# Kernel optimization log

Measured on AMD Instinct MI355X. Metric: run time of the kernel, lower is better.

The kernel has to match this reference:

```python
import jax, jax.numpy as jnp
import numpy as np

E = 1024  # embedding_size
H = 16    # multi_head_num


def setup_inputs() -> dict:
    key = jax.random.key(0)
    ks = jax.random.split(key, 9)
    B, N = 4, 1024
    s = 1.0 / np.sqrt(E)
    return {
        "x": jax.random.normal(ks[0], (B, N, E), dtype=jnp.float32),
        "Wq": jax.random.normal(ks[1], (E, E), dtype=jnp.float32) * s,
        "bq": jax.random.normal(ks[2], (E,), dtype=jnp.float32) * 0.02,
        "Wk": jax.random.normal(ks[3], (E, E), dtype=jnp.float32) * s,
        "bk": jax.random.normal(ks[4], (E,), dtype=jnp.float32) * 0.02,
        "Wv": jax.random.normal(ks[5], (E, E), dtype=jnp.float32) * s,
        "bv": jax.random.normal(ks[6], (E,), dtype=jnp.float32) * 0.02,
        "Wo": jax.random.normal(ks[7], (E, E), dtype=jnp.float32) * s,
        "bo": jax.random.normal(ks[8], (E,), dtype=jnp.float32) * 0.02,
    }


def reference(x, Wq, bq, Wk, bk, Wv, bv, Wo, bo):
    B, N, _ = x.shape
    d = E // H

    def heads(y):  # [B,N,E] -> [B,H,N,d]
        return y.reshape(B, N, H, d).transpose(0, 2, 1, 3)

    q = heads(x @ Wq.T + bq)
    k = heads(x @ Wk.T + bk)
    v = heads(x @ Wv.T + bv)

    energy = jnp.einsum('bhqd,bhkd->bhqk', q, k)
    # NOTE: module divides by sqrt(E) AFTER softmax (faithful to source)
    scaling = jnp.asarray(E, x.dtype) ** 0.5
    att = jax.nn.softmax(energy, axis=-1) / scaling
    out = jnp.einsum('bhal,bhlv->bhav', att, v)
    out = out.transpose(0, 2, 1, 3).reshape(B, N, E)
    return out @ Wo.T + bo
```

## Files before the change

### kernel.cpp

```cpp
#include <hip/hip_runtime.h>
#include <hip/hip_bf16.h>


typedef __bf16 bf16x8 __attribute__((ext_vector_type(8)));
typedef __bf16 bf16x4 __attribute__((ext_vector_type(4)));
typedef float  f32x4  __attribute__((ext_vector_type(4)));

#define LOG2E 1.44269504f

__device__ __forceinline__ void glds16(const __bf16* g, __bf16* l) {
  __builtin_amdgcn_global_load_lds(
      (const __attribute__((address_space(1))) void*)g,
      (__attribute__((address_space(3))) void*)l, 16, 0, 0);
}

__global__ __launch_bounds__(256) void cvt_f32_bf16(const float* __restrict__ in,
                                                    __bf16* __restrict__ out, int n4) {
  int i = blockIdx.x * 256 + threadIdx.x;
  if (i < n4) {
    float4 v = *(const float4*)(in + (size_t)i * 4);
    bf16x4 b = {(__bf16)v.x, (__bf16)v.y, (__bf16)v.z, (__bf16)v.w};
    *(bf16x4*)(out + (size_t)i * 4) = b;
  }
}

__global__ __launch_bounds__(256) void cvt_all(const float* __restrict__ x,
                                               const float* __restrict__ Wq,
                                               const float* __restrict__ Wk,
                                               const float* __restrict__ Wv,
                                               const float* __restrict__ Wo,
                                               __bf16* __restrict__ xb,
                                               __bf16* __restrict__ Wqb,
                                               __bf16* __restrict__ Wkb,
                                               __bf16* __restrict__ Wvb,
                                               __bf16* __restrict__ Wob) {
  const int i = blockIdx.x * 256 + threadIdx.x;
  const float* src;
  __bf16* dst;
  int off;
  if (i < 1048576) {
    src = x; dst = xb; off = i;
  } else {
    const int j = i - 1048576;
    const int seg = j >> 18;
    off = j & 262143;
    src = (seg == 0) ? Wq : (seg == 1) ? Wk : (seg == 2) ? Wv : Wo;
    dst = (seg == 0) ? Wqb : (seg == 1) ? Wkb : (seg == 2) ? Wvb : Wob;
  }
  float4 v = *(const float4*)(src + (size_t)off * 4);
  bf16x4 b = {(__bf16)v.x, (__bf16)v.y, (__bf16)v.z, (__bf16)v.w};
  *(bf16x4*)(dst + (size_t)off * 4) = b;
}

template <bool WBF16>
__global__ __launch_bounds__(256, 3) void gemm_qkv(const __bf16* __restrict__ A,
                                                   const void* __restrict__ Wqp,
                                                   const void* __restrict__ Wkp,
                                                   const void* __restrict__ Wvp,
                                                   const float* __restrict__ bq,
                                                   const float* __restrict__ bk,
                                                   const float* __restrict__ bv,
                                                   __bf16* __restrict__ Qw,
                                                   __bf16* __restrict__ Kw,
                                                   __bf16* __restrict__ Vw) {
  constexpr int BST = WBF16 ? 64 : 72;
  __shared__ __attribute__((aligned(16))) __bf16 As[128][64];
  __shared__ __attribute__((aligned(16))) __bf16 Bs[128 * BST];

  const int tid = threadIdx.x;
  const int lane = tid & 63, w = tid >> 6;
  const int wm = w >> 1, wn = w & 1;
  const int l15 = lane & 15, lq = lane >> 4;
  const int lr = lane >> 3, lc = lane & 7;
  const int xs = l15 & 7;

  const int bid = blockIdx.x;
  const int c = bid & 7, t = bid >> 3;
  const int z = t >> 5;
  const int r = t & 31;
  const int nb = r & 7;
  const int mb = c * 4 + (r >> 3);
  const int m0 = mb * 128, n0 = nb * 128;

  const void* Wp = (z == 0) ? Wqp : (z == 1) ? Wkp : Wvp;
  const float* bias = (z == 0) ? bq : (z == 1) ? bk : bv;
  __bf16* C = (z == 0) ? Qw : (z == 1) ? Kw : Vw;
  const float scale = (z == 0) ? LOG2E : 1.0f;

  f32x4 acc[4][4] = {};

  for (int k0 = 0; k0 < 1024; k0 += 64) {
#pragma unroll
    for (int i = 0; i < 4; ++i) {
      const int row = w * 32 + i * 8 + lr;
      glds16(A + (size_t)(m0 + row) * 1024 + k0 + ((lc ^ lr) * 8), &As[row][lc * 8]);
    }
    if (WBF16) {
      const __bf16* Wb = (const __bf16*)Wp;
#pragma unroll
      for (int i = 0; i < 4; ++i) {
        const int row = w * 32 + i * 8 + lr;
        glds16(Wb + (size_t)(n0 + row) * 1024 + k0 + ((lc ^ lr) * 8), &Bs[row * 64 + lc * 8]);
      }
    } else {
      const float* W = (const float*)Wp;
#pragma unroll
      for (int i = 0; i < 8; ++i) {
        const int cc = i * 256 + tid, row = cc >> 4, col = (cc & 15) * 4;
        float4 wv = *(const float4*)(W + (size_t)(n0 + row) * 1024 + k0 + col);
        bf16x4 b4 = {(__bf16)wv.x, (__bf16)wv.y, (__bf16)wv.z, (__bf16)wv.w};
        *(bf16x4*)(&Bs[row * 72 + col]) = b4;
      }
    }
    __syncthreads();
#pragma unroll
    for (int s = 0; s < 2; ++s) {
      bf16x8 af[4], bfv[4];
#pragma unroll
      for (int mt = 0; mt < 4; ++mt)
        af[mt] = *(const bf16x8*)(&As[wm * 64 + mt * 16 + l15][((s * 4 + lq) ^ xs) * 8]);
#pragma unroll
      for (int nt = 0; nt < 4; ++nt) {
        const int row = wn * 64 + nt * 16 + l15;
        if (WBF16)
          bfv[nt] = *(const bf16x8*)(&Bs[row * 64 + (((s * 4 + lq) ^ xs) * 8)]);
        else
          bfv[nt] = *(const bf16x8*)(&Bs[row * 72 + s * 32 + lq * 8]);
      }
#pragma unroll
      for (int mt = 0; mt < 4; ++mt)
#pragma unroll
        for (int nt = 0; nt < 4; ++nt)
          acc[mt][nt] = __builtin_amdgcn_mfma_f32_16x16x32_bf16(
              af[mt], bfv[nt], acc[mt][nt], 0, 0, 0);
    }
    __syncthreads();
  }

#pragma unroll
  for (int mt = 0; mt < 4; ++mt) {
    const int mg_base = m0 + wm * 64 + mt * 16 + lq * 4;
    const int bb = mg_base >> 10, nr0 = mg_base & 1023;
#pragma unroll
    for (int nt = 0; nt < 4; ++nt) {
      const int ng = n0 + wn * 64 + nt * 16 + l15;
      const float bv = bias[ng];
      const int h = ng >> 6, dd = ng & 63;
      if (z != 2) {
#pragma unroll
        for (int rr = 0; rr < 4; ++rr) {
          const int mg = mg_base + rr;
          const size_t idx =
              ((size_t)(bb * 16 + h) << 16) + (size_t)(mg & 1023) * 64 + dd;
          C[idx] = (__bf16)((acc[mt][nt][rr] + bv) * scale);
        }
      } else {
        bf16x4 o4 = {(__bf16)(acc[mt][nt][0] + bv), (__bf16)(acc[mt][nt][1] + bv),
                     (__bf16)(acc[mt][nt][2] + bv), (__bf16)(acc[mt][nt][3] + bv)};
        *(bf16x4*)(&C[((size_t)(bb * 16 + h) << 16) + (size_t)dd * 1024 + nr0]) = o4;
      }
    }
  }
}

__global__ __launch_bounds__(256, 2) void gemm_out(const __bf16* __restrict__ A,
                                                   const __bf16* __restrict__ W,
                                                   const float* __restrict__ bias,
                                                   float* __restrict__ C) {
  extern __shared__ __attribute__((aligned(16))) __bf16 lds_o[];
  __bf16(*As)[64][64] = (__bf16(*)[64][64])lds_o;
  __bf16(*Bs)[128][64] = (__bf16(*)[128][64])(lds_o + 12288);

  const int tid = threadIdx.x;
  const int lane = tid & 63, w = tid >> 6;
  const int wm = w >> 1, wn = w & 1;
  const int l15 = lane & 15, lq = lane >> 4;
  const int lr = lane >> 3, lc = lane & 7;
  const int xs = l15 & 7;

  const int bid = blockIdx.x;
  const int c = bid & 7, t = bid >> 3;
  const int mb = c * 8 + (t & 7);
  const int nb = t >> 3;
  const int m0 = mb * 64, n0 = nb * 128;

  auto stage = [&](int kb, int sl) {
    const int k0 = kb * 64;
#pragma unroll
    for (int i = 0; i < 2; ++i) {
      const int row = w * 16 + i * 8 + lr;
      glds16(A + (size_t)(m0 + row) * 1024 + k0 + ((lc ^ lr) * 8), &As[sl][row][lc * 8]);
    }
#pragma unroll
    for (int i = 0; i < 4; ++i) {
      const int row = w * 32 + i * 8 + lr;
      glds16(W + (size_t)(n0 + row) * 1024 + k0 + ((lc ^ lr) * 8), &Bs[sl][row][lc * 8]);
    }
  };

  f32x4 acc[2][4] = {};

  stage(0, 0);
  stage(1, 1);

  for (int kb = 0; kb < 16; ++kb) {
    if (kb < 15)
      asm volatile("s_waitcnt vmcnt(6)" ::: "memory");
    else
      asm volatile("s_waitcnt vmcnt(0)" ::: "memory");
    __builtin_amdgcn_s_barrier();
    if (kb < 14) stage(kb + 2, (kb + 2) % 3);

    const int sl = kb % 3;
#pragma unroll
    for (int s = 0; s < 2; ++s) {
      bf16x8 af[2], bfv[4];
#pragma unroll
      for (int mt = 0; mt < 2; ++mt)
        af[mt] = *(const bf16x8*)(&As[sl][wm * 32 + mt * 16 + l15][((s * 4 + lq) ^ xs) * 8]);
#pragma unroll
      for (int nt = 0; nt < 4; ++nt)
        bfv[nt] = *(const bf16x8*)(&Bs[sl][wn * 64 + nt * 16 + l15][((s * 4 + lq) ^ xs) * 8]);
      __builtin_amdgcn_s_setprio(1);
#pragma unroll
      for (int mt = 0; mt < 2; ++mt)
#pragma unroll
        for (int nt = 0; nt < 4; ++nt)
          acc[mt][nt] = __builtin_amdgcn_mfma_f32_16x16x32_bf16(
              af[mt], bfv[nt], acc[mt][nt], 0, 0, 0);
      __builtin_amdgcn_s_setprio(0);
    }
  }

#pragma unroll
  for (int mt = 0; mt < 2; ++mt) {
    const int mg_base = m0 + wm * 32 + mt * 16 + lq * 4;
#pragma unroll
    for (int nt = 0; nt < 4; ++nt) {
      const int ng = n0 + wn * 64 + nt * 16 + l15;
      const float bv = bias[ng];
#pragma unroll
      for (int r = 0; r < 4; ++r)
        C[(size_t)(mg_base + r) * 1024 + ng] = acc[mt][nt][r] + bv;
    }
  }
}

__global__ __launch_bounds__(256, 2) void attn_kernel(const __bf16* __restrict__ Q,
                                                      const __bf16* __restrict__ K,
                                                      const __bf16* __restrict__ Vt,
                                                      __bf16* __restrict__ O) {
  extern __shared__ __attribute__((aligned(16))) __bf16 lds_a[];
  __bf16(*Ks)[64][64] = (__bf16(*)[64][64])lds_a;
  __bf16(*Vs)[64][64] = (__bf16(*)[64][64])(lds_a + 12288);
  __bf16* PQ = lds_a + 24576;
  __bf16(*Qst)[64] = (__bf16(*)[64])PQ;
  __bf16(*Ps)[32][72] = (__bf16(*)[32][72])PQ;

  const int tid = threadIdx.x;
  const int lane = tid & 63, w = tid >> 6;
  const int l15 = lane & 15, lq = lane >> 4;
  const int lr = lane >> 3, lc = lane & 7;
  const int xs = l15 & 7;

  const int bh = blockIdx.x;
  const int qt = blockIdx.y;
  const __bf16* Qh = Q + (size_t)bh * 65536;
  const __bf16* Kh = K + (size_t)bh * 65536;
  const __bf16* Vh = Vt + (size_t)bh * 65536;

  auto stage_kv = [&](int kb, int sl) {
#pragma unroll
    for (int i = 0; i < 2; ++i) {
      const int row = w * 16 + i * 8 + lr;
      glds16(Kh + (size_t)kb * 4096 + (size_t)row * 64 + ((lc ^ lr) * 8),
             &Ks[sl][row][lc * 8]);
      glds16(Vh + (size_t)row * 1024 + kb * 64 + ((lc ^ lr) * 8),
             &Vs[sl][row][lc * 8]);
    }
  };

#pragma unroll
  for (int i = 0; i < 4; ++i) {
    const int row = w * 32 + i * 8 + lr;
    glds16(Qh + (size_t)(qt * 128 + row) * 64 + ((lc ^ lr) * 8), &Qst[row][lc * 8]);
  }
  stage_kv(0, 0);
  __syncthreads();
  bf16x8 bqr[2][2];
#pragma unroll
  for (int nq = 0; nq < 2; ++nq)
#pragma unroll
    for (int s = 0; s < 2; ++s)
      bqr[nq][s] = *(const bf16x8*)(&Qst[w * 32 + nq * 16 + l15][((s * 4 + lq) ^ xs) * 8]);
  __syncthreads();
  stage_kv(1, 1);

  float l_run[2] = {0.0f, 0.0f};
  f32x4 oacc[2][4] = {};

  for (int kb = 0; kb < 16; ++kb) {
    if (kb < 15)
      asm volatile("s_waitcnt vmcnt(4)" ::: "memory");
    else
      asm volatile("s_waitcnt vmcnt(0)" ::: "memory");
    __builtin_amdgcn_s_barrier();
    if (kb < 14) stage_kv(kb + 2, (kb + 2) % 3);
    const int sl = kb % 3;

    f32x4 sacc[2][4] = {};
    __builtin_amdgcn_s_setprio(1);
#pragma unroll
    for (int s = 0; s < 2; ++s) {
#pragma unroll
      for (int mt = 0; mt < 4; ++mt) {
        bf16x8 ak = *(const bf16x8*)(&Ks[sl][mt * 16 + l15][((s * 4 + lq) ^ xs) * 8]);
#pragma unroll
        for (int nq = 0; nq < 2; ++nq)
          sacc[nq][mt] = __builtin_amdgcn_mfma_f32_16x16x32_bf16(
              ak, bqr[nq][s], sacc[nq][mt], 0, 0, 0);
      }
    }
    __builtin_amdgcn_s_setprio(0);

#pragma unroll
    for (int nq = 0; nq < 2; ++nq) {
      float sum = 0.0f;
#pragma unroll
      for (int mt = 0; mt < 4; ++mt)
#pragma unroll
        for (int r = 0; r < 4; ++r) {
          const float e = __builtin_amdgcn_exp2f(sacc[nq][mt][r]);
          sacc[nq][mt][r] = e;
          sum += e;
        }
      sum += __shfl_xor(sum, 16, 64);
      sum += __shfl_xor(sum, 32, 64);
      l_run[nq] += sum;
    }

#pragma unroll
    for (int nq = 0; nq < 2; ++nq)
#pragma unroll
      for (int mt = 0; mt < 4; ++mt) {
        bf16x4 p4 = {(__bf16)sacc[nq][mt][0], (__bf16)sacc[nq][mt][1],
                     (__bf16)sacc[nq][mt][2], (__bf16)sacc[nq][mt][3]};
        *(bf16x4*)(&Ps[w][nq * 16 + l15][mt * 16 + lq * 4]) = p4;
      }
    __threadfence_block();

    __builtin_amdgcn_s_setprio(1);
#pragma unroll
    for (int s = 0; s < 2; ++s) {
      bf16x8 bp[2];
#pragma unroll
      for (int nq = 0; nq < 2; ++nq)
        bp[nq] = *(const bf16x8*)(&Ps[w][nq * 16 + l15][s * 32 + lq * 8]);
#pragma unroll
      for (int mt = 0; mt < 4; ++mt) {
        bf16x8 av = *(const bf16x8*)(&Vs[sl][mt * 16 + l15][((s * 4 + lq) ^ xs) * 8]);
#pragma unroll
        for (int nq = 0; nq < 2; ++nq)
          oacc[nq][mt] = __builtin_amdgcn_mfma_f32_16x16x32_bf16(
              av, bp[nq], oacc[nq][mt], 0, 0, 0);
      }
    }
    __builtin_amdgcn_s_setprio(0);
  }

  const int b = bh >> 4, h = bh & 15;
#pragma unroll
  for (int nq = 0; nq < 2; ++nq) {
    const float inv = 1.0f / (l_run[nq] * 32.0f);
    const size_t base =
        (size_t)(b * 1024 + qt * 128 + w * 32 + nq * 16 + l15) * 1024 + h * 64;
#pragma unroll
    for (int mt = 0; mt < 4; ++mt) {
      bf16x4 o4 = {(__bf16)(oacc[nq][mt][0] * inv), (__bf16)(oacc[nq][mt][1] * inv),
                   (__bf16)(oacc[nq][mt][2] * inv), (__bf16)(oacc[nq][mt][3] * inv)};
      *(bf16x4*)(&O[base + mt * 16 + lq * 4]) = o4;
    }
  }
}

extern "C" void kernel_launch(void* const* d_in, const int* in_sizes, int n_in,
                              void* d_out, int out_size, void* d_ws, size_t ws_size,
                              hipStream_t stream) {
  const float* x  = (const float*)d_in[0];
  const float* Wq = (const float*)d_in[1];
  const float* bq = (const float*)d_in[2];
  const float* Wk = (const float*)d_in[3];
  const float* bk = (const float*)d_in[4];
  const float* Wv = (const float*)d_in[5];
  const float* bv = (const float*)d_in[6];
  const float* Wo = (const float*)d_in[7];
  const float* bo = (const float*)d_in[8];
  float* out = (float*)d_out;

  const size_t SZ = (size_t)4 * 1024 * 1024;
  __bf16* Qw = (__bf16*)d_ws;
  __bf16* Kw = Qw + SZ;
  __bf16* Vw = Kw + SZ;
  __bf16* s3 = Vw + SZ;
  __bf16* xb = s3;
  __bf16* Ow = s3;

  dim3 blk(256);

  static bool attr_set = false;
  if (!attr_set) {
    (void)hipFuncSetAttribute((const void*)attn_kernel,
                              hipFuncAttributeMaxDynamicSharedMemorySize, 67584);
    (void)hipFuncSetAttribute((const void*)gemm_out,
                              hipFuncAttributeMaxDynamicSharedMemorySize, 73728);
    attr_set = true;
  }

  if (ws_size >= (size_t)40 * 1024 * 1024) {
    __bf16* Wqb = s3 + SZ;
    __bf16* Wkb = Wqb + SZ / 4;
    __bf16* Wvb = Wkb + SZ / 4;
    __bf16* Wob = Wvb + SZ / 4;
    cvt_all<<<8192, blk, 0, stream>>>(x, Wq, Wk, Wv, Wo, xb, Wqb, Wkb, Wvb, Wob);
    gemm_qkv<true><<<dim3(768), blk, 0, stream>>>(xb, Wqb, Wkb, Wvb,
                                                  bq, bk, bv, Qw, Kw, Vw);
    attn_kernel<<<dim3(64, 8), blk, 67584, stream>>>(Qw, Kw, Vw, Ow);
    gemm_out<<<dim3(512), blk, 73728, stream>>>(Ow, Wob, bo, out);
  } else {
    __bf16* Wob = Kw;
    cvt_f32_bf16<<<4096, blk, 0, stream>>>(x, xb, 1048576);
    gemm_qkv<false><<<dim3(768), blk, 0, stream>>>(xb, Wq, Wk, Wv,
                                                   bq, bk, bv, Qw, Kw, Vw);
    attn_kernel<<<dim3(64, 8), blk, 67584, stream>>>(Qw, Kw, Vw, Ow);
    cvt_f32_bf16<<<1024, blk, 0, stream>>>(Wo, Wob, 262144);
    gemm_out<<<dim3(512), blk, 73728, stream>>>(Ow, Wob, bo, out);
  }
}
```

Before: 161.1 us.

## Replace QKV GEMM with 256x192-tile 512-thread kernel with staged async LDS pipeline

Adds a new fused QKV projection kernel that uses 256x192 output tiles with 8 waves and 128x48 per-wave subtiles. A/B tiles are loaded with direct global-to-LDS loads into a double-buffered A and triple-buffered B ring, with loads interleaved among MFMA phases and s_setprio. The grid shrinks from 768 to 256 blocks to get more operand reuse per tile. In exchange it uses about 136KB of LDS per block and has fewer blocks than some GPUs have CUs, which risks underfilling the device and adds extra barriers.

```diff
diff --git a/kernel.cpp b/kernel.cpp
--- a/kernel.cpp
+++ b/kernel.cpp
@@ -52,6 +52,131 @@
   *(bf16x4*)(dst + (size_t)off * 4) = b;
 }
 
+__global__ __launch_bounds__(512, 2) void gemm_qkv9(const __bf16* __restrict__ A,
+                                                    const __bf16* __restrict__ Wqp,
+                                                    const __bf16* __restrict__ Wkp,
+                                                    const __bf16* __restrict__ Wvp,
+                                                    const float* __restrict__ bq,
+                                                    const float* __restrict__ bk,
+                                                    const float* __restrict__ bv,
+                                                    __bf16* __restrict__ Qw,
+                                                    __bf16* __restrict__ Kw,
+                                                    __bf16* __restrict__ Vw) {
+  extern __shared__ __attribute__((aligned(16))) __bf16 lds[];
+
+  const int tid = threadIdx.x;
+  const int lane = tid & 63;
+  const int w = tid >> 6, wm = w >> 2, wn = w & 3;
+  const int l15 = lane & 15, lq = lane >> 4;
+  const int xs = l15 & 7;
+  const int srow = tid >> 3;
+  const int scol = tid & 7;
+  const int sxor = (scol ^ (srow & 7)) * 8;
+
+  const int bid = blockIdx.x;
+  const int c = bid & 7, t = bid >> 3;
+  const int mb = c * 2 + (t & 1);
+  const int nb = t >> 1;
+  const int m0 = mb * 256;
+  const int n0g = nb * 192;
+
+  auto stageA = [&](int T, int chunk) {
+    const int row = chunk * 64 + srow;
+    glds16(A + (size_t)(m0 + row) * 1024 + T * 64 + sxor,
+           lds + (T & 1) * 16384 + row * 64 + scol * 8);
+  };
+  auto stageB = [&](int T, int chunk) {
+    const int row = chunk * 64 + srow;
+    const int g = n0g + row;
+    const int z = g >> 10;
+    const __bf16* W = (z == 0) ? Wqp : (z == 1) ? Wkp : Wvp;
+    glds16(W + (size_t)(g & 1023) * 1024 + T * 64 + sxor,
+           lds + 32768 + (T % 3) * 12288 + row * 64 + scol * 8);
+  };
+
+  f32x4 acc[8][3] = {};
+
+#pragma unroll
+  for (int ch = 0; ch < 3; ++ch) stageB(0, ch);
+#pragma unroll
+  for (int ch = 0; ch < 4; ++ch) stageA(0, ch);
+#pragma unroll
+  for (int ch = 0; ch < 3; ++ch) stageB(1, ch);
+
+  for (int T = 0; T < 16; ++T) {
+    if (T < 15)
+      asm volatile("s_waitcnt vmcnt(3)" ::: "memory");
+    else
+      asm volatile("s_waitcnt vmcnt(0)" ::: "memory");
+    __builtin_amdgcn_s_barrier();
+
+    const __bf16* Ab = lds + (T & 1) * 16384 + (wm * 128) * 64;
+    const __bf16* Bb = lds + 32768 + (T % 3) * 12288 + (wn * 48) * 64;
+
+#pragma unroll
+    for (int p = 0; p < 4; ++p) {
+      const int s = p >> 1, mh = p & 1;
+      const int kc = ((s * 4 + lq) ^ xs) * 8;
+      bf16x8 af[4], bf[3];
+#pragma unroll
+      for (int mt = 0; mt < 4; ++mt)
+        af[mt] = *(const bf16x8*)(Ab + (mh * 64 + mt * 16 + l15) * 64 + kc);
+#pragma unroll
+      for (int nt = 0; nt < 3; ++nt)
+        bf[nt] = *(const bf16x8*)(Bb + (nt * 16 + l15) * 64 + kc);
+
+      if (T < 15) {
+        if (p == 0)      { stageA(T + 1, 0); stageA(T + 1, 1); }
+        else if (p == 1) { stageA(T + 1, 2); stageA(T + 1, 3); }
+        else if (T < 14) {
+          if (p == 2)    { stageB(T + 2, 0); stageB(T + 2, 1); }
+          else           { stageB(T + 2, 2); }
+        }
+      }
+
+      __builtin_amdgcn_s_barrier();
+      __builtin_amdgcn_s_setprio(1);
+#pragma unroll
+      for (int mt = 0; mt < 4; ++mt)
+#pragma unroll
+        for (int nt = 0; nt < 3; ++nt)
+          acc[mh * 4 + mt][nt] = __builtin_amdgcn_mfma_f32_16x16x32_bf16(
+              af[mt], bf[nt], acc[mh * 4 + mt][nt], 0, 0, 0);
+      __builtin_amdgcn_s_setprio(0);
+      __builtin_amdgcn_s_barrier();
+    }
+  }
+
+#pragma unroll
+  for (int mt = 0; mt < 8; ++mt) {
+    const int mg_base = m0 + wm * 128 + mt * 16 + lq * 4;
+    const int bb = mg_base >> 10, nr0 = mg_base & 1023;
+#pragma unroll
+    for (int nt = 0; nt < 3; ++nt) {
+      const int ng = n0g + wn * 48 + nt * 16 + l15;
+      const int z = ng >> 10, nl = ng & 1023;
+      const float* bias = (z == 0) ? bq : (z == 1) ? bk : bv;
+      __bf16* C = (z == 0) ? Qw : (z == 1) ? Kw : Vw;
+      const float scale = (z == 0) ? LOG2E : 1.0f;
+      const float bv4 = bias[nl];
+      const int h = nl >> 6, dd = nl & 63;
+      if (z != 2) {
+#pragma unroll
+        for (int rr = 0; rr < 4; ++rr) {
+          const int mg = mg_base + rr;
+          const size_t idx =
+              ((size_t)(bb * 16 + h) << 16) + (size_t)(mg & 1023) * 64 + dd;
+          C[idx] = (__bf16)((acc[mt][nt][rr] + bv4) * scale);
+        }
+      } else {
+        bf16x4 o4 = {(__bf16)(acc[mt][nt][0] + bv4), (__bf16)(acc[mt][nt][1] + bv4),
+                     (__bf16)(acc[mt][nt][2] + bv4), (__bf16)(acc[mt][nt][3] + bv4)};
+        *(bf16x4*)(&C[((size_t)(bb * 16 + h) << 16) + (size_t)dd * 1024 + nr0]) = o4;
+      }
+    }
+  }
+}
+
 template <bool WBF16>
 __global__ __launch_bounds__(256, 3) void gemm_qkv(const __bf16* __restrict__ A,
                                                    const void* __restrict__ Wqp,
@@ -409,6 +534,8 @@
 
   static bool attr_set = false;
   if (!attr_set) {
+    (void)hipFuncSetAttribute((const void*)gemm_qkv9,
+                              hipFuncAttributeMaxDynamicSharedMemorySize, 139264);
     (void)hipFuncSetAttribute((const void*)attn_kernel,
                               hipFuncAttributeMaxDynamicSharedMemorySize, 67584);
     (void)hipFuncSetAttribute((const void*)gemm_out,
@@ -422,8 +549,8 @@
     __bf16* Wvb = Wkb + SZ / 4;
     __bf16* Wob = Wvb + SZ / 4;
     cvt_all<<<8192, blk, 0, stream>>>(x, Wq, Wk, Wv, Wo, xb, Wqb, Wkb, Wvb, Wob);
-    gemm_qkv<true><<<dim3(768), blk, 0, stream>>>(xb, Wqb, Wkb, Wvb,
-                                                  bq, bk, bv, Qw, Kw, Vw);
+    gemm_qkv9<<<dim3(256), dim3(512), 139264, stream>>>(xb, Wqb, Wkb, Wvb,
+                                                        bq, bk, bv, Qw, Kw, Vw);
     attn_kernel<<<dim3(64, 8), blk, 67584, stream>>>(Qw, Kw, Vw, Ow);
     gemm_out<<<dim3(512), blk, 73728, stream>>>(Ow, Wob, bo, out);
   } else {
```

After: 189.5 us. 17.7% more time.
